# Performance work log

Hardware: AMD Instinct MI355X
Metric: run time of the kernel (lower is better)

The kernel has to match this reference:

```python
import jax, jax.numpy as jnp
import numpy as np

# config matching init_kwargs
C = 256; G = 16; GC = C // G; K = 3; P = K * K
PAD = 1; STR = 1; DIL = 1; OFFSET_SCALE = 1.0
N, H, W = 8, 64, 64


def setup_inputs() -> dict:
    key = jax.random.key(0)
    ks = jax.random.split(key, 8)
    def rn(k, shape, sc):
        return jax.random.normal(k, shape, jnp.float32) * sc
    return {
        "x": jax.random.normal(ks[0], (N, H, W, C), jnp.float32),
        "dw_w": rn(ks[1], (C, 1, K, K), 0.1),          # depthwise conv weight (OIHW, groups=C)
        "dw_b": jnp.zeros((C,), jnp.float32),
        "ln_g": jnp.ones((C,), jnp.float32),
        "ln_b": jnp.zeros((C,), jnp.float32),
        "off_w": rn(ks[2], (G * P * 2, C), 0.01),      # offset head (small so offsets stay sane)
        "off_b": jnp.zeros((G * P * 2,), jnp.float32),
        "mask_w": rn(ks[3], (G * P, C), 0.01),
        "mask_b": jnp.zeros((G * P,), jnp.float32),
        "in_w": rn(ks[4], (C, C), 0.05),
        "in_b": jnp.zeros((C,), jnp.float32),
        "out_w": rn(ks[5], (C, C), 0.05),
        "out_b": jnp.zeros((C,), jnp.float32),
    }


def _layer_norm(x, g, b, eps=1e-6):
    m = x.mean(-1, keepdims=True)
    v = ((x - m) ** 2).mean(-1, keepdims=True)
    return (x - m) * jax.lax.rsqrt(v + eps) * g + b


def _grid_sample_bilinear(img, grid):
    # img: (B, Cc, Hh, Ww); grid: (B, L, P, 2) normalized to [-1, 1], (x, y) order.
    # Matches torch.grid_sample(mode='bilinear', padding_mode='zeros', align_corners=False).
    B, Cc, Hh, Ww = img.shape
    gx = (grid[..., 0] + 1.0) * (Ww * 0.5) - 0.5
    gy = (grid[..., 1] + 1.0) * (Hh * 0.5) - 0.5
    x0 = jnp.floor(gx); y0 = jnp.floor(gy)
    tx = gx - x0; ty = gy - y0
    img_f = img.reshape(B, Cc, Hh * Ww)
    def corner(xi, yi, w):
        valid = (xi >= 0) & (xi < Ww) & (yi >= 0) & (yi < Hh)
        idx = (jnp.clip(yi, 0, Hh - 1) * Ww + jnp.clip(xi, 0, Ww - 1)).astype(jnp.int32)
        v = jnp.take_along_axis(img_f, idx.reshape(B, 1, -1), axis=2)  # (B, Cc, L*P)
        return v * (w * valid).reshape(B, 1, -1)
    out = (corner(x0, y0, (1 - tx) * (1 - ty)) + corner(x0 + 1, y0, tx * (1 - ty))
           + corner(x0, y0 + 1, (1 - tx) * ty) + corner(x0 + 1, y0 + 1, tx * ty))
    return out.reshape(B, Cc, grid.shape[1], grid.shape[2])  # (B, Cc, L, P)


def _dcnv3_core(x, offset, mask):
    # x: (N,H,W,C) value features; offset: (N,H,W,G*P*2); mask: (N,H,W,G*P)
    xpad = jnp.pad(x, ((0, 0), (PAD, PAD), (PAD, PAD), (0, 0)))
    Hi, Wi = H + 2 * PAD, W + 2 * PAD
    Ho, Wo = H, W
    # reference points (centers of receptive field), normalized by padded size
    start = (DIL * (K - 1)) // 2 + 0.5
    ry = (start + jnp.arange(Ho, dtype=jnp.float32) * STR) / Hi
    rx = (start + jnp.arange(Wo, dtype=jnp.float32) * STR) / Wi
    ref = jnp.stack([jnp.broadcast_to(rx[None, :], (Ho, Wo)),
                     jnp.broadcast_to(ry[:, None], (Ho, Wo))], -1)  # (Ho,Wo,2) (x,y)
    # dilation grid, x-major flattening to match torch meshgrid('ij') ordering
    d = jnp.arange(K, dtype=jnp.float32) * DIL - (DIL * (K - 1)) // 2
    kgrid = jnp.stack([jnp.repeat(d, K) / Wi, jnp.tile(d, K) / Hi], -1)  # (P,2)
    off = offset.reshape(N, Ho, Wo, G, P, 2)
    norm = jnp.array([Wi, Hi], jnp.float32)
    loc = (ref[None, :, :, None, None, :]
           + kgrid[None, None, None, None, :, :] * OFFSET_SCALE
           + off * OFFSET_SCALE / norm)                      # (N,Ho,Wo,G,P,2)
    sg = (2.0 * loc - 1.0).reshape(N, Ho * Wo, G, P, 2)
    sg = sg.transpose(0, 2, 1, 3, 4).reshape(N * G, Ho * Wo, P, 2)
    val = xpad.reshape(N, Hi * Wi, G * GC).transpose(0, 2, 1).reshape(N * G, GC, Hi, Wi)
    samp = _grid_sample_bilinear(val, sg)                    # (N*G, GC, Ho*Wo, P)
    m = mask.reshape(N, Ho * Wo, G, P).transpose(0, 2, 1, 3).reshape(N * G, 1, Ho * Wo, P)
    out = (samp * m).sum(-1)                                 # (N*G, GC, Ho*Wo)
    return out.reshape(N, G * GC, Ho * Wo).transpose(0, 2, 1).reshape(N, Ho, Wo, C)


def reference(x, dw_w, dw_b, ln_g, ln_b, off_w, off_b, mask_w, mask_b, in_w, in_b, out_w, out_b):
    xp = x @ in_w.T + in_b                                   # input_proj (values)
    # depthwise conv -> LN (channels_last) -> exact GELU
    y = jax.lax.conv_general_dilated(
        x.transpose(0, 3, 1, 2), dw_w, (1, 1), ((PAD, PAD), (PAD, PAD)),
        feature_group_count=C, dimension_numbers=('NCHW', 'OIHW', 'NCHW'))
    y = y + dw_b[None, :, None, None]
    x1 = jax.nn.gelu(_layer_norm(y.transpose(0, 2, 3, 1), ln_g, ln_b), approximate=False)
    offset = x1 @ off_w.T + off_b                            # (N,H,W,G*P*2)
    mlogits = (x1 @ mask_w.T + mask_b).reshape(N, H, W, G, P)
    mask = jax.nn.softmax(mlogits, axis=-1).reshape(N, H, W, G * P)
    out = _dcnv3_core(xp, offset, mask)
    return out @ out_w.T + out_b
```

## Files before the change

### kernel.cpp

```cpp
#include <hip/hip_runtime.h>


#define LL 32768
#define CC 256

typedef __bf16 bf16;
typedef __bf16 bf16x4 __attribute__((ext_vector_type(4)));
typedef __bf16 bf16x8 __attribute__((ext_vector_type(8)));
typedef float f32x4v __attribute__((ext_vector_type(4)));
typedef float f32x2 __attribute__((ext_vector_type(2)));

__device__ __forceinline__ void gload16(const bf16* g, const bf16* lds_base) {
    __builtin_amdgcn_global_load_lds(
        (const __attribute__((address_space(1))) void*)g,
        (__attribute__((address_space(3))) void*)lds_base, 16, 0, 0);
}

__global__ __launch_bounds__(256) void k_prep(
    const float* __restrict__ in_w, const float* __restrict__ off_w,
    const float* __restrict__ mask_w, const float* __restrict__ out_w,
    const float* __restrict__ dw_w, const float* __restrict__ off_b,
    const float* __restrict__ mask_b,
    bf16* __restrict__ in_h, bf16* __restrict__ hw_h,
    bf16* __restrict__ out_h,
    float* __restrict__ dwT, float* __restrict__ hbias) {
    int idx = blockIdx.x * 256 + threadIdx.x;
    if (idx < 60416) {
        const float* s; bf16* hi; int i;
        if (idx < 16384)      { s = in_w;   hi = in_h;          i = idx; }
        else if (idx < 34816) { s = off_w;  hi = hw_h;          i = idx - 16384; }
        else if (idx < 44032) { s = mask_w; hi = hw_h + 73728;  i = idx - 34816; }
        else                  { s = out_w;  hi = out_h;         i = idx - 44032; }
        float4 v = *(const float4*)(s + (size_t)i * 4);
        bf16x4 h;
        h[0] = (bf16)v.x; h[1] = (bf16)v.y; h[2] = (bf16)v.z; h[3] = (bf16)v.w;
        *(bf16x4*)(hi + (size_t)i * 4) = h;
    } else if (idx < 62720) {
        int e = idx - 60416;
        int c = e & 255, j = e >> 8;
        dwT[j * 256 + c] = dw_w[c * 9 + j];
    } else if (idx < 63232) {
        int e = idx - 62720;
        hbias[e] = (e < 288) ? off_b[e] : (e < 432 ? mask_b[e - 288] : 0.f);
    } else if (idx < 68352) {
        int e = idx - 63232;
        bf16x4 z = {(bf16)0.f, (bf16)0.f, (bf16)0.f, (bf16)0.f};
        *(bf16x4*)(hw_h + 110592 + (size_t)e * 4) = z;
    }
}

__global__ __launch_bounds__(256) void k_dwln(
    const float* __restrict__ x, const float* __restrict__ dwT,
    const float* __restrict__ dw_b, const float* __restrict__ ln_g,
    const float* __restrict__ ln_b, bf16* __restrict__ x1h,
    bf16* __restrict__ xb) {
    int t = threadIdx.x;
    int q = t >> 6, u = t & 63;
    int l = blockIdx.x * 4 + q;
    int w = l & 63, h = (l >> 6) & 63, n = l >> 12;
    int c0 = u * 4;

    float4 acc = *(const float4*)(dw_b + c0);
    float4 xc = {0.f, 0.f, 0.f, 0.f};
#pragma unroll
    for (int kh = 0; kh < 3; ++kh) {
        int hh = h + kh - 1;
        if (hh < 0 || hh >= 64) continue;
#pragma unroll
        for (int kw = 0; kw < 3; ++kw) {
            int ww = w + kw - 1;
            if (ww < 0 || ww >= 64) continue;
            float4 xv = *(const float4*)(x + (size_t)(((n * 64 + hh) * 64) + ww) * CC + c0);
            if (kh == 1 && kw == 1) xc = xv;
            float4 wv = *(const float4*)(dwT + (kh * 3 + kw) * 256 + c0);
            acc.x += xv.x * wv.x; acc.y += xv.y * wv.y;
            acc.z += xv.z * wv.z; acc.w += xv.w * wv.w;
        }
    }
    bf16x4 xcb;
    xcb[0] = (bf16)xc.x; xcb[1] = (bf16)xc.y;
    xcb[2] = (bf16)xc.z; xcb[3] = (bf16)xc.w;
    *(bf16x4*)(xb + (size_t)l * CC + c0) = xcb;

    float s = acc.x + acc.y + acc.z + acc.w;
    float ss = acc.x * acc.x + acc.y * acc.y + acc.z * acc.z + acc.w * acc.w;
#pragma unroll
    for (int d = 1; d < 64; d <<= 1) {
        s += __shfl_xor(s, d);
        ss += __shfl_xor(ss, d);
    }
    float mean = s * (1.0f / 256.0f);
    float var = ss * (1.0f / 256.0f) - mean * mean;
    float rstd = rsqrtf(var + 1e-6f);
    float4 gv = *(const float4*)(ln_g + c0);
    float4 bv = *(const float4*)(ln_b + c0);
    float xn0 = (acc.x - mean) * rstd * gv.x + bv.x;
    float xn1 = (acc.y - mean) * rstd * gv.y + bv.y;
    float xn2 = (acc.z - mean) * rstd * gv.z + bv.z;
    float xn3 = (acc.w - mean) * rstd * gv.w + bv.w;
    bf16x4 oh;
    oh[0] = (bf16)(0.5f * xn0 * (1.0f + erff(xn0 * 0.70710678118654752f)));
    oh[1] = (bf16)(0.5f * xn1 * (1.0f + erff(xn1 * 0.70710678118654752f)));
    oh[2] = (bf16)(0.5f * xn2 * (1.0f + erff(xn2 * 0.70710678118654752f)));
    oh[3] = (bf16)(0.5f * xn3 * (1.0f + erff(xn3 * 0.70710678118654752f)));
    *(bf16x4*)(x1h + (size_t)l * CC + c0) = oh;
}

template <bool OBF16>
__device__ __forceinline__ void gemm_core(
    const bf16* __restrict__ A, const bf16* __restrict__ Wh,
    const float* __restrict__ bias, float* __restrict__ C32,
    bf16* __restrict__ Cbf, int Nout, int mb, int nb) {
    int t = threadIdx.x, wave = t >> 6, lane = t & 63;
    int wm = wave & 1, wn = wave >> 1;
    int fm = lane & 15, fq = lane >> 4;

    __shared__ bf16 smem[16384];

    const bf16* gbase[4];
    int lofs[4];
#pragma unroll
    for (int j = 0; j < 4; ++j) {
        int seg = wave * 4 + j;
        int arr = seg >> 3;
        int row = (seg & 7) * 16 + (lane >> 2);
        int col = (lane & 3) * 8;
        gbase[j] = (arr == 0) ? (A + (size_t)(mb + row) * CC + col)
                              : (Wh + (size_t)(nb + row) * CC + col);
        lofs[j] = seg * 512;
    }

    f32x4v acc[4][4];
#pragma unroll
    for (int i = 0; i < 4; ++i)
#pragma unroll
        for (int j = 0; j < 4; ++j) acc[i][j] = (f32x4v){0.f, 0.f, 0.f, 0.f};

#pragma unroll
    for (int j = 0; j < 4; ++j) gload16(gbase[j], smem + lofs[j]);

    for (int kt = 0; kt < 8; ++kt) {
        const bf16* buf = smem + (kt & 1) * 8192;
        bf16* nxt = smem + ((kt & 1) ^ 1) * 8192;
        __syncthreads();
        if (kt < 7) {
#pragma unroll
            for (int j = 0; j < 4; ++j)
                gload16(gbase[j] + (kt + 1) * 32, nxt + lofs[j]);
        }
        bf16x8 af[4], bfh[4];
#pragma unroll
        for (int i = 0; i < 4; ++i)
            af[i] = *(const bf16x8*)&buf[(wm * 64 + i * 16 + fm) * 32 + fq * 8];
#pragma unroll
        for (int j = 0; j < 4; ++j)
            bfh[j] = *(const bf16x8*)&buf[4096 + (wn * 64 + j * 16 + fm) * 32 + fq * 8];
#pragma unroll
        for (int i = 0; i < 4; ++i)
#pragma unroll
            for (int j = 0; j < 4; ++j)
                acc[i][j] = __builtin_amdgcn_mfma_f32_16x16x32_bf16(
                    af[i], bfh[j], acc[i][j], 0, 0, 0);
    }

#pragma unroll
    for (int j = 0; j < 4; ++j) {
        int n_g = nb + wn * 64 + j * 16 + fm;
        if (n_g >= Nout) continue;
        float bv = bias[n_g];
#pragma unroll
        for (int i = 0; i < 4; ++i) {
            int m_g = mb + wm * 64 + i * 16 + fq * 4;
#pragma unroll
            for (int rg = 0; rg < 4; ++rg) {
                float o = acc[i][j][rg] + bv;
                if (OBF16)
                    Cbf[(size_t)(m_g + rg) * Nout + n_g] = (bf16)o;
                else
                    C32[(size_t)(m_g + rg) * Nout + n_g] = o;
            }
        }
    }
}

template <bool OBF16>
__global__ __launch_bounds__(256) void k_gemm(
    const bf16* __restrict__ A, const bf16* __restrict__ Wh,
    const float* __restrict__ bias, float* __restrict__ C32,
    bf16* __restrict__ Cbf, int Nout) {
    gemm_core<OBF16>(A, Wh, bias, C32, Cbf, Nout,
                     blockIdx.x * 128, blockIdx.y * 128);
}

__global__ __launch_bounds__(256) void k_gemm_ih(
    const bf16* __restrict__ xb, const bf16* __restrict__ x1h,
    const bf16* __restrict__ in_h, const bf16* __restrict__ hw_h,
    const float* __restrict__ in_b, const float* __restrict__ hbias,
    bf16* __restrict__ xpb, bf16* __restrict__ headb) {
    int mb = blockIdx.x * 128;
    int y = blockIdx.y;
    const bf16 *A, *W;
    const float* bs;
    bf16* Cb;
    int Nout, nb;
    if (y < 2) { A = xb;  W = in_h; bs = in_b;  Cb = xpb;   Nout = 256; nb = y * 128; }
    else       { A = x1h; W = hw_h; bs = hbias; Cb = headb; Nout = 432; nb = (y - 2) * 128; }
    gemm_core<true>(A, W, bs, nullptr, Cb, Nout, mb, nb);
}

__device__ __forceinline__ void mac8(f32x2 acc[4], bf16x8 v, float wt) {
    union { bf16x8 b; unsigned u[4]; } cu;
    cu.b = v;
    f32x2 wv = {wt, wt};
#pragma unroll
    for (int i = 0; i < 4; ++i) {
        f32x2 a;
        a.x = __uint_as_float(cu.u[i] << 16);
        a.y = __uint_as_float(cu.u[i] & 0xffff0000u);
        acc[i] += a * wv;
    }
}

__global__ __launch_bounds__(256) void k_gather(
    const bf16* __restrict__ xp, const bf16* __restrict__ head,
    bf16* __restrict__ rows) {
    int t = threadIdx.x;
    int q = t >> 5, u = t & 31;
    int l = blockIdx.x * 8 + q;
    int w = l & 63, h = (l >> 6) & 63, n = l >> 12;

    __shared__ float CW[8][576];
    __shared__ int BASE[8][144];

    for (int j = u; j < 432; j += 32) CW[q][j] = (float)head[(size_t)l * 432 + j];
    __syncthreads();

    if (u < 16) {
        int g = u;
        float mx = -1e30f;
#pragma unroll
        for (int p = 0; p < 9; ++p) mx = fmaxf(mx, CW[q][288 + g * 9 + p]);
        float s = 0.f, e[9];
#pragma unroll
        for (int p = 0; p < 9; ++p) { e[p] = expf(CW[q][288 + g * 9 + p] - mx); s += e[p]; }
        float inv = 1.0f / s;
#pragma unroll
        for (int p = 0; p < 9; ++p) CW[q][288 + g * 9 + p] = e[p] * inv;
    }
    __syncthreads();

    float4 cwr[5];
    int baser[5];
#pragma unroll
    for (int k = 0; k < 5; ++k) {
        if (k < 4 || u < 16) {
            int ei = u + 32 * k;
            int g = ei / 9, p = ei - g * 9;
            float ox = CW[q][g * 18 + p * 2 + 0];
            float oy = CW[q][g * 18 + p * 2 + 1];
            float m  = CW[q][288 + ei];
            float ax = (float)(w + (p / 3) - 1) + ox;
            float ay = (float)(h + (p % 3) - 1) + oy;
            float x0f = floorf(ax), y0f = floorf(ay);
            int x0 = (int)x0f, y0 = (int)y0f;
            float tx = ax - x0f, ty = ay - y0f;
            int xb, yb;
            float wxa, wxb, wya, wyb;
            if (x0 < 0)       { xb = 0;  wxa = (x0 == -1) ? tx : 0.f; wxb = 0.f; }
            else if (x0 > 62) { xb = 62; wxa = 0.f; wxb = (x0 == 63) ? (1.f - tx) : 0.f; }
            else              { xb = x0; wxa = 1.f - tx; wxb = tx; }
            if (y0 < 0)       { yb = 0;  wya = (y0 == -1) ? ty : 0.f; wyb = 0.f; }
            else if (y0 > 62) { yb = 62; wya = 0.f; wyb = (y0 == 63) ? (1.f - ty) : 0.f; }
            else              { yb = y0; wya = 1.f - ty; wyb = ty; }
            float4 cw;
            cw.x = m * wxa * wya; cw.y = m * wxb * wya;
            cw.z = m * wxa * wyb; cw.w = m * wxb * wyb;
            cwr[k] = cw;
            baser[k] = (n << 20) + (yb * 64 + xb) * 256;
        }
    }
    __syncthreads();
#pragma unroll
    for (int k = 0; k < 5; ++k) {
        if (k < 4 || u < 16) {
            int ei = u + 32 * k;
            *(float4*)&CW[q][ei * 4] = cwr[k];
            BASE[q][ei] = baser[k];
        }
    }
    __syncthreads();

    int g = u >> 1;
    int c0 = g * 16 + (u & 1) * 8;
    const bf16* xpc = xp + c0;
    f32x2 acc[4];
    acc[0] = (f32x2){0.f, 0.f}; acc[1] = (f32x2){0.f, 0.f};
    acc[2] = (f32x2){0.f, 0.f}; acc[3] = (f32x2){0.f, 0.f};
#pragma unroll
    for (int p = 0; p < 9; ++p) {
        int ei = g * 9 + p;
        float4 cw = *(const float4*)&CW[q][ei * 4];
        int base = BASE[q][ei];
        const bf16* p0 = xpc + base;
        const bf16* p1 = p0 + 16384;
        bf16x8 v00 = *(const bf16x8*)(p0);
        bf16x8 v01 = *(const bf16x8*)(p0 + 256);
        bf16x8 v10 = *(const bf16x8*)(p1);
        bf16x8 v11 = *(const bf16x8*)(p1 + 256);
        mac8(acc, v00, cw.x);
        mac8(acc, v01, cw.y);
        mac8(acc, v10, cw.z);
        mac8(acc, v11, cw.w);
    }
    bf16x8 oh;
    oh[0] = (bf16)acc[0].x; oh[1] = (bf16)acc[0].y;
    oh[2] = (bf16)acc[1].x; oh[3] = (bf16)acc[1].y;
    oh[4] = (bf16)acc[2].x; oh[5] = (bf16)acc[2].y;
    oh[6] = (bf16)acc[3].x; oh[7] = (bf16)acc[3].y;
    *(bf16x8*)(rows + (size_t)l * CC + c0) = oh;
}

__device__ __forceinline__ float dot256f(const float* a, const float* wrow) {
    const float4* w4 = (const float4*)wrow;
    float s = 0.f;
#pragma unroll 16
    for (int i = 0; i < 64; ++i) {
        float4 u = w4[i];
        const float* ap = a + i * 4;
        s += ap[0] * u.x + ap[1] * u.y + ap[2] * u.z + ap[3] * u.w;
    }
    return s;
}

__global__ __launch_bounds__(256) void k_inproj_fb(
    const float* __restrict__ x, const float* __restrict__ in_w,
    const float* __restrict__ in_b, float* __restrict__ xp) {
    int l = blockIdx.x;
    int t = threadIdx.x;
    __shared__ float xa[256];
    xa[t] = x[l * CC + t];
    __syncthreads();
    xp[l * CC + t] = dot256f(xa, in_w + t * CC) + in_b[t];
}

__device__ __forceinline__ float fetch_px_fb(const float* base, int yy, int xx) {
    if (xx < 0 || xx >= 64 || yy < 0 || yy >= 64) return 0.f;
    return base[(yy * 64 + xx) * CC];
}

__global__ __launch_bounds__(256) void k_main_fb(
    const float* __restrict__ x, const float* __restrict__ xp,
    const float* __restrict__ dw_w, const float* __restrict__ dw_b,
    const float* __restrict__ ln_g, const float* __restrict__ ln_b,
    const float* __restrict__ off_w, const float* __restrict__ off_b,
    const float* __restrict__ mask_w, const float* __restrict__ mask_b,
    const float* __restrict__ out_w, const float* __restrict__ out_b,
    float* __restrict__ out) {
    int l = blockIdx.x;
    int t = threadIdx.x;
    int w = l & 63, h = (l >> 6) & 63, n = l >> 12;
    __shared__ float x1[256];
    __shared__ float red[256];
    __shared__ float offs[288];
    __shared__ float ms[144];
    __shared__ float row[256];

    float acc = dw_b[t];
#pragma unroll
    for (int kh = 0; kh < 3; ++kh) {
        int hh = h + kh - 1;
        if (hh < 0 || hh >= 64) continue;
#pragma unroll
        for (int kw = 0; kw < 3; ++kw) {
            int ww = w + kw - 1;
            if (ww < 0 || ww >= 64) continue;
            acc += x[(((n * 64 + hh) * 64) + ww) * CC + t] * dw_w[t * 9 + kh * 3 + kw];
        }
    }
    red[t] = acc;
    __syncthreads();
    for (int s = 128; s > 0; s >>= 1) {
        if (t < s) red[t] += red[t + s];
        __syncthreads();
    }
    float mean = red[0] * (1.0f / 256.0f);
    __syncthreads();
    float d = acc - mean;
    red[t] = d * d;
    __syncthreads();
    for (int s = 128; s > 0; s >>= 1) {
        if (t < s) red[t] += red[t + s];
        __syncthreads();
    }
    float var = red[0] * (1.0f / 256.0f);
    float xn = d * rsqrtf(var + 1e-6f) * ln_g[t] + ln_b[t];
    x1[t] = 0.5f * xn * (1.0f + erff(xn * 0.70710678118654752f));
    __syncthreads();

    offs[t] = dot256f(x1, off_w + t * CC) + off_b[t];
    if (t < 32) {
        int j = 256 + t;
        offs[j] = dot256f(x1, off_w + j * CC) + off_b[j];
    }
    if (t < 144) ms[t] = dot256f(x1, mask_w + t * CC) + mask_b[t];
    __syncthreads();

    if (t < 16) {
        int g = t;
        float mx = -1e30f;
#pragma unroll
        for (int p = 0; p < 9; ++p) mx = fmaxf(mx, ms[g * 9 + p]);
        float s = 0.f, e[9];
#pragma unroll
        for (int p = 0; p < 9; ++p) { e[p] = expf(ms[g * 9 + p] - mx); s += e[p]; }
        float inv = 1.0f / s;
#pragma unroll
        for (int p = 0; p < 9; ++p) ms[g * 9 + p] = e[p] * inv;
    }
    __syncthreads();

    int g = t >> 4;
    const float* base = xp + (size_t)n * 64 * 64 * CC + t;
    float acc2 = 0.f;
#pragma unroll
    for (int p = 0; p < 9; ++p) {
        float ox = offs[g * 18 + p * 2 + 0];
        float oy = offs[g * 18 + p * 2 + 1];
        float ax = (float)(w + (p / 3) - 1) + ox;
        float ay = (float)(h + (p % 3) - 1) + oy;
        float x0f = floorf(ax), y0f = floorf(ay);
        int x0 = (int)x0f, y0 = (int)y0f;
        float tx = ax - x0f, ty = ay - y0f;
        float v00 = fetch_px_fb(base, y0, x0);
        float v01 = fetch_px_fb(base, y0, x0 + 1);
        float v10 = fetch_px_fb(base, y0 + 1, x0);
        float v11 = fetch_px_fb(base, y0 + 1, x0 + 1);
        float bl = (v00 * (1.f - tx) + v01 * tx) * (1.f - ty) +
                   (v10 * (1.f - tx) + v11 * tx) * ty;
        acc2 += ms[g * 9 + p] * bl;
    }
    row[t] = acc2;
    __syncthreads();
    out[l * CC + t] = dot256f(row, out_w + t * CC) + out_b[t];
}

extern "C" void kernel_launch(void* const* d_in, const int* in_sizes, int n_in,
                              void* d_out, int out_size, void* d_ws,
                              size_t ws_size, hipStream_t stream) {
    const float* x      = (const float*)d_in[0];
    const float* dw_w   = (const float*)d_in[1];
    const float* dw_b   = (const float*)d_in[2];
    const float* ln_g   = (const float*)d_in[3];
    const float* ln_b   = (const float*)d_in[4];
    const float* off_w  = (const float*)d_in[5];
    const float* off_b  = (const float*)d_in[6];
    const float* mask_w = (const float*)d_in[7];
    const float* mask_b = (const float*)d_in[8];
    const float* in_w   = (const float*)d_in[9];
    const float* in_b   = (const float*)d_in[10];
    const float* out_w  = (const float*)d_in[11];
    const float* out_b  = (const float*)d_in[12];
    float* out = (float*)d_out;

    const size_t szBF    = (size_t)LL * CC * 2;
    const size_t szHEADB = (size_t)LL * 432 * 2;
    const size_t szWB    = 1048576;
    const size_t need    = 3 * szBF + szHEADB + szWB;

    dim3 blk(256);
    if (ws_size >= need) {
        char* p = (char*)d_ws;
        bf16* x1h = (bf16*)p; p += szBF;
        bf16* xpb = (bf16*)p; p += szBF;
        bf16* xb  = (bf16*)p; p += szBF;
        bf16* headb = (bf16*)p; p += szHEADB;
        bf16* in_h  = (bf16*)p; p += 131072;
        bf16* hw_h  = (bf16*)p; p += 262144;
        bf16* out_h = (bf16*)p; p += 131072;
        float* dwT  = (float*)p; p += 9216;
        float* hbias = (float*)p;
        bf16* rows = x1h;

        k_prep<<<dim3(267), blk, 0, stream>>>(in_w, off_w, mask_w, out_w, dw_w,
                                              off_b, mask_b, in_h, hw_h, out_h,
                                              dwT, hbias);
        k_dwln<<<dim3(LL / 4), blk, 0, stream>>>(x, dwT, dw_b, ln_g, ln_b, x1h, xb);
        k_gemm_ih<<<dim3(256, 6), blk, 0, stream>>>(
            xb, x1h, in_h, hw_h, in_b, hbias, xpb, headb);
        k_gather<<<dim3(LL / 8), blk, 0, stream>>>(xpb, headb, rows);
        k_gemm<false><<<dim3(256, 2), blk, 0, stream>>>(
            rows, out_h, out_b, out, nullptr, 256);
    } else {
        float* xp = (float*)d_ws;
        k_inproj_fb<<<dim3(LL), blk, 0, stream>>>(x, in_w, in_b, xp);
        k_main_fb<<<dim3(LL), blk, 0, stream>>>(x, xp, dw_w, dw_b, ln_g, ln_b,
                                                off_w, off_b, mask_w, mask_b,
                                                out_w, out_b, out);
    }
}
```

Baseline: 199.1 us.

## Stage neighbourhood window of xp in LDS for deformable gather

Each gather block now copies a 6-row by 12-pixel window of the bf16 value tensor around its 8 output pixels into shared memory with global_load_lds. Bilinear samples whose corners fall inside this window are read from LDS; the rest fall back to global loads, flagged by bit-inverting the stored base offset. The head rows are also loaded as 16-byte vectors instead of scalars. The aim is to cut repeated global and L2 traffic for overlapping sample footprints, at the cost of roughly 36 KB more LDS per block, which lowers occupancy, plus window loads near image borders that can fall outside the buffer.

```diff
diff --git a/kernel.cpp b/kernel.cpp
--- a/kernel.cpp
+++ b/kernel.cpp
@@ -226,13 +226,42 @@
     bf16* __restrict__ rows) {
     int t = threadIdx.x;
     int q = t >> 5, u = t & 31;
-    int l = blockIdx.x * 8 + q;
+    int bl = blockIdx.x * 8;
+    int l = bl + q;
     int w = l & 63, h = (l >> 6) & 63, n = l >> 12;
-
+    int c0 = bl & 63;
+    int r  = (bl >> 6) & 63;
+    int nb = bl >> 12;
+
+    __shared__ bf16 WIN[18432];
     __shared__ float CW[8][576];
     __shared__ int BASE[8][144];
 
-    for (int j = u; j < 432; j += 32) CW[q][j] = (float)head[(size_t)l * 432 + j];
+    {
+        const char* xpB = (const char*)xp;
+        long long orig = (long long)((nb * 64 + (r - 2)) * 64 + (c0 - 2)) * 512;
+#pragma unroll
+        for (int j = 0; j < 9; ++j) {
+            int chunk = t + 256 * j;
+            int wr = chunk / 384;
+            int cx = chunk - wr * 384;
+            const char* src = xpB + orig + (long long)wr * 32768 + (long long)cx * 16;
+            gload16((const bf16*)src, WIN + chunk * 8);
+        }
+    }
+#pragma unroll
+    for (int jj = 0; jj < 2; ++jj) {
+        int cj = t + jj * 256;
+        if (cj < 432) {
+            int px = cj / 54, j = cj - px * 54;
+            bf16x8 v = *(const bf16x8*)(head + (size_t)(bl + px) * 432 + j * 8);
+            float4 f0, f1;
+            f0.x = (float)v[0]; f0.y = (float)v[1]; f0.z = (float)v[2]; f0.w = (float)v[3];
+            f1.x = (float)v[4]; f1.y = (float)v[5]; f1.z = (float)v[6]; f1.w = (float)v[7];
+            *(float4*)&CW[px][j * 8] = f0;
+            *(float4*)&CW[px][j * 8 + 4] = f1;
+        }
+    }
     __syncthreads();
 
     if (u < 16) {
@@ -264,19 +293,26 @@
             float x0f = floorf(ax), y0f = floorf(ay);
             int x0 = (int)x0f, y0 = (int)y0f;
             float tx = ax - x0f, ty = ay - y0f;
-            int xb, yb;
+            int xb_, yb_;
             float wxa, wxb, wya, wyb;
-            if (x0 < 0)       { xb = 0;  wxa = (x0 == -1) ? tx : 0.f; wxb = 0.f; }
-            else if (x0 > 62) { xb = 62; wxa = 0.f; wxb = (x0 == 63) ? (1.f - tx) : 0.f; }
-            else              { xb = x0; wxa = 1.f - tx; wxb = tx; }
-            if (y0 < 0)       { yb = 0;  wya = (y0 == -1) ? ty : 0.f; wyb = 0.f; }
-            else if (y0 > 62) { yb = 62; wya = 0.f; wyb = (y0 == 63) ? (1.f - ty) : 0.f; }
-            else              { yb = y0; wya = 1.f - ty; wyb = ty; }
+            if (x0 < 0)       { xb_ = 0;  wxa = (x0 == -1) ? tx : 0.f; wxb = 0.f; }
+            else if (x0 > 62) { xb_ = 62; wxa = 0.f; wxb = (x0 == 63) ? (1.f - tx) : 0.f; }
+            else              { xb_ = x0; wxa = 1.f - tx; wxb = tx; }
+            if (y0 < 0)       { yb_ = 0;  wya = (y0 == -1) ? ty : 0.f; wyb = 0.f; }
+            else if (y0 > 62) { yb_ = 62; wya = 0.f; wyb = (y0 == 63) ? (1.f - ty) : 0.f; }
+            else              { yb_ = y0; wya = 1.f - ty; wyb = ty; }
             float4 cw;
             cw.x = m * wxa * wya; cw.y = m * wxb * wya;
             cw.z = m * wxa * wyb; cw.w = m * wxb * wyb;
             cwr[k] = cw;
-            baser[k] = (n << 20) + (yb * 64 + xb) * 256;
+            bool inWin = (xb_ >= c0 - 2) & (xb_ <= c0 + 8) &
+                         (yb_ >= r - 2) & (yb_ <= r + 2);
+            if (inWin) {
+                int slot = (yb_ - (r - 2)) * 12 + (xb_ - (c0 - 2));
+                baser[k] = slot * 256 + g * 16;
+            } else {
+                baser[k] = ~((n << 20) + (yb_ * 64 + xb_) * 256);
+            }
         }
     }
     __syncthreads();
@@ -290,23 +326,34 @@
     }
     __syncthreads();
 
-    int g = u >> 1;
-    int c0 = g * 16 + (u & 1) * 8;
-    const bf16* xpc = xp + c0;
+    int g2 = u >> 1;
+    int half = u & 1;
+    int c0ch = g2 * 16 + half * 8;
+    const bf16* xpc = xp + c0ch;
     f32x2 acc[4];
     acc[0] = (f32x2){0.f, 0.f}; acc[1] = (f32x2){0.f, 0.f};
     acc[2] = (f32x2){0.f, 0.f}; acc[3] = (f32x2){0.f, 0.f};
 #pragma unroll
     for (int p = 0; p < 9; ++p) {
-        int ei = g * 9 + p;
+        int ei = g2 * 9 + p;
         float4 cw = *(const float4*)&CW[q][ei * 4];
-        int base = BASE[q][ei];
-        const bf16* p0 = xpc + base;
-        const bf16* p1 = p0 + 16384;
-        bf16x8 v00 = *(const bf16x8*)(p0);
-        bf16x8 v01 = *(const bf16x8*)(p0 + 256);
-        bf16x8 v10 = *(const bf16x8*)(p1);
-        bf16x8 v11 = *(const bf16x8*)(p1 + 256);
+        int b = BASE[q][ei];
+        bf16x8 v00, v01, v10, v11;
+        if (b >= 0) {
+            int e0 = b + half * 8;
+            v00 = *(const bf16x8*)&WIN[e0];
+            v01 = *(const bf16x8*)&WIN[e0 + 256];
+            v10 = *(const bf16x8*)&WIN[e0 + 3072];
+            v11 = *(const bf16x8*)&WIN[e0 + 3328];
+        } else {
+            int idxe = ~b;
+            const bf16* p0 = xpc + idxe;
+            const bf16* p1 = p0 + 16384;
+            v00 = *(const bf16x8*)(p0);
+            v01 = *(const bf16x8*)(p0 + 256);
+            v10 = *(const bf16x8*)(p1);
+            v11 = *(const bf16x8*)(p1 + 256);
+        }
         mac8(acc, v00, cw.x);
         mac8(acc, v01, cw.y);
         mac8(acc, v10, cw.z);
@@ -317,7 +364,7 @@
     oh[2] = (bf16)acc[1].x; oh[3] = (bf16)acc[1].y;
     oh[4] = (bf16)acc[2].x; oh[5] = (bf16)acc[2].y;
     oh[6] = (bf16)acc[3].x; oh[7] = (bf16)acc[3].y;
-    *(bf16x8*)(rows + (size_t)l * CC + c0) = oh;
+    *(bf16x8*)(rows + (size_t)l * CC + c0ch) = oh;
 }
 
 __device__ __forceinline__ float dot256f(const float* a, const float* wrow) {
```

Result: slower. 214.9 us (+8.0%).

## Store projected values in group-major layout for gather locality

Applied to the files above, without the earlier changes.

The input-projection GEMM now writes its bf16 output in a group-major layout (n, group, pixel, 16 channels) instead of pixel-major rows of 256 channels. The deformable gather kernel computes addresses in this layout, so a group's four bilinear corners sit in a compact 32-byte-per-pixel plane and neighbouring pixels are 32 bytes apart rather than 512. The aim is better cache-line and L2 locality for the random gathers. The cost is scattered 2-byte stores in the GEMM epilogue, which may write less efficiently.

```diff
diff --git a/kernel.cpp b/kernel.cpp
--- a/kernel.cpp
+++ b/kernel.cpp
@@ -106,7 +106,7 @@
     *(bf16x4*)(x1h + (size_t)l * CC + c0) = oh;
 }
 
-template <bool OBF16>
+template <bool OBF16, bool GM>
 __device__ __forceinline__ void gemm_core(
     const bf16* __restrict__ A, const bf16* __restrict__ Wh,
     const float* __restrict__ bias, float* __restrict__ C32,
@@ -174,10 +174,18 @@
 #pragma unroll
             for (int rg = 0; rg < 4; ++rg) {
                 float o = acc[i][j][rg] + bv;
-                if (OBF16)
-                    Cbf[(size_t)(m_g + rg) * Nout + n_g] = (bf16)o;
-                else
+                if (OBF16) {
+                    if (GM) {
+                        int mg = m_g + rg;
+                        size_t idx = ((size_t)((mg >> 12) * 16 + (n_g >> 4)) * 4096
+                                      + (mg & 4095)) * 16 + (n_g & 15);
+                        Cbf[idx] = (bf16)o;
+                    } else {
+                        Cbf[(size_t)(m_g + rg) * Nout + n_g] = (bf16)o;
+                    }
+                } else {
                     C32[(size_t)(m_g + rg) * Nout + n_g] = o;
+                }
             }
         }
     }
@@ -188,8 +196,8 @@
     const bf16* __restrict__ A, const bf16* __restrict__ Wh,
     const float* __restrict__ bias, float* __restrict__ C32,
     bf16* __restrict__ Cbf, int Nout) {
-    gemm_core<OBF16>(A, Wh, bias, C32, Cbf, Nout,
-                     blockIdx.x * 128, blockIdx.y * 128);
+    gemm_core<OBF16, false>(A, Wh, bias, C32, Cbf, Nout,
+                            blockIdx.x * 128, blockIdx.y * 128);
 }
 
 __global__ __launch_bounds__(256) void k_gemm_ih(
@@ -199,13 +207,11 @@
     bf16* __restrict__ xpb, bf16* __restrict__ headb) {
     int mb = blockIdx.x * 128;
     int y = blockIdx.y;
-    const bf16 *A, *W;
-    const float* bs;
-    bf16* Cb;
-    int Nout, nb;
-    if (y < 2) { A = xb;  W = in_h; bs = in_b;  Cb = xpb;   Nout = 256; nb = y * 128; }
-    else       { A = x1h; W = hw_h; bs = hbias; Cb = headb; Nout = 432; nb = (y - 2) * 128; }
-    gemm_core<true>(A, W, bs, nullptr, Cb, Nout, mb, nb);
+    if (y < 2)
+        gemm_core<true, true>(xb, in_h, in_b, nullptr, xpb, 256, mb, y * 128);
+    else
+        gemm_core<true, false>(x1h, hw_h, hbias, nullptr, headb, 432, mb,
+                               (y - 2) * 128);
 }
 
 __device__ __forceinline__ void mac8(f32x2 acc[4], bf16x8 v, float wt) {
@@ -276,7 +282,7 @@
             cw.x = m * wxa * wya; cw.y = m * wxb * wya;
             cw.z = m * wxa * wyb; cw.w = m * wxb * wyb;
             cwr[k] = cw;
-            baser[k] = (n << 20) + (yb * 64 + xb) * 256;
+            baser[k] = ((n * 16 + g) * 4096 + yb * 64 + xb) * 16;
         }
     }
     __syncthreads();
@@ -291,8 +297,8 @@
     __syncthreads();
 
     int g = u >> 1;
-    int c0 = g * 16 + (u & 1) * 8;
-    const bf16* xpc = xp + c0;
+    int half = u & 1;
+    int goff = half * 8;
     f32x2 acc[4];
     acc[0] = (f32x2){0.f, 0.f}; acc[1] = (f32x2){0.f, 0.f};
     acc[2] = (f32x2){0.f, 0.f}; acc[3] = (f32x2){0.f, 0.f};
@@ -300,13 +306,11 @@
     for (int p = 0; p < 9; ++p) {
         int ei = g * 9 + p;
         float4 cw = *(const float4*)&CW[q][ei * 4];
-        int base = BASE[q][ei];
-        const bf16* p0 = xpc + base;
-        const bf16* p1 = p0 + 16384;
+        const bf16* p0 = xp + BASE[q][ei] + goff;
         bf16x8 v00 = *(const bf16x8*)(p0);
-        bf16x8 v01 = *(const bf16x8*)(p0 + 256);
-        bf16x8 v10 = *(const bf16x8*)(p1);
-        bf16x8 v11 = *(const bf16x8*)(p1 + 256);
+        bf16x8 v01 = *(const bf16x8*)(p0 + 16);
+        bf16x8 v10 = *(const bf16x8*)(p0 + 1024);
+        bf16x8 v11 = *(const bf16x8*)(p0 + 1040);
         mac8(acc, v00, cw.x);
         mac8(acc, v01, cw.y);
         mac8(acc, v10, cw.z);
@@ -317,7 +321,7 @@
     oh[2] = (bf16)acc[1].x; oh[3] = (bf16)acc[1].y;
     oh[4] = (bf16)acc[2].x; oh[5] = (bf16)acc[2].y;
     oh[6] = (bf16)acc[3].x; oh[7] = (bf16)acc[3].y;
-    *(bf16x8*)(rows + (size_t)l * CC + c0) = oh;
+    *(bf16x8*)(rows + (size_t)l * CC + g * 16 + goff) = oh;
 }
 
 __device__ __forceinline__ float dot256f(const float* a, const float* wrow) {
```

Measured after the change: 212.3 us. +6.6%, slower.

## Fuse weight prep into depthwise-LN kernel and use smaller-M tile output GEMM

Applied to the files above, without the earlier changes.

Merges the weight-conversion prep kernel into the depthwise conv + LayerNorm kernel by appending extra blocks, which removes one launch and the dwT transpose. The conv now reads the OIHW depthwise weights directly with strided scalar loads. The final output GEMM moves to a dedicated kernel with 64x128 tiles, doubling the block count for better CU occupancy. Risks: the scalar strided weight loads are less coalesced than the old float4 reads from the transposed buffer, and the prep blocks now share the launch with the conv blocks.

```diff
diff --git a/kernel.cpp b/kernel.cpp
--- a/kernel.cpp
+++ b/kernel.cpp
@@ -16,52 +16,48 @@
         (__attribute__((address_space(3))) void*)lds_base, 16, 0, 0);
 }
 
-__global__ __launch_bounds__(256) void k_prep(
+__global__ __launch_bounds__(256) void k_dwp(
+    const float* __restrict__ x, const float* __restrict__ dw_w,
+    const float* __restrict__ dw_b, const float* __restrict__ ln_g,
+    const float* __restrict__ ln_b, bf16* __restrict__ x1h,
+    bf16* __restrict__ xb,
     const float* __restrict__ in_w, const float* __restrict__ off_w,
     const float* __restrict__ mask_w, const float* __restrict__ out_w,
-    const float* __restrict__ dw_w, const float* __restrict__ off_b,
-    const float* __restrict__ mask_b,
+    const float* __restrict__ off_b, const float* __restrict__ mask_b,
     bf16* __restrict__ in_h, bf16* __restrict__ hw_h,
-    bf16* __restrict__ out_h,
-    float* __restrict__ dwT, float* __restrict__ hbias) {
-    int idx = blockIdx.x * 256 + threadIdx.x;
-    if (idx < 60416) {
-        const float* s; bf16* hi; int i;
-        if (idx < 16384)      { s = in_w;   hi = in_h;          i = idx; }
-        else if (idx < 34816) { s = off_w;  hi = hw_h;          i = idx - 16384; }
-        else if (idx < 44032) { s = mask_w; hi = hw_h + 73728;  i = idx - 34816; }
-        else                  { s = out_w;  hi = out_h;         i = idx - 44032; }
-        float4 v = *(const float4*)(s + (size_t)i * 4);
-        bf16x4 h;
-        h[0] = (bf16)v.x; h[1] = (bf16)v.y; h[2] = (bf16)v.z; h[3] = (bf16)v.w;
-        *(bf16x4*)(hi + (size_t)i * 4) = h;
-    } else if (idx < 62720) {
-        int e = idx - 60416;
-        int c = e & 255, j = e >> 8;
-        dwT[j * 256 + c] = dw_w[c * 9 + j];
-    } else if (idx < 63232) {
-        int e = idx - 62720;
-        hbias[e] = (e < 288) ? off_b[e] : (e < 432 ? mask_b[e - 288] : 0.f);
-    } else if (idx < 68352) {
-        int e = idx - 63232;
-        bf16x4 z = {(bf16)0.f, (bf16)0.f, (bf16)0.f, (bf16)0.f};
-        *(bf16x4*)(hw_h + 110592 + (size_t)e * 4) = z;
-    }
-}
-
-__global__ __launch_bounds__(256) void k_dwln(
-    const float* __restrict__ x, const float* __restrict__ dwT,
-    const float* __restrict__ dw_b, const float* __restrict__ ln_g,
-    const float* __restrict__ ln_b, bf16* __restrict__ x1h,
-    bf16* __restrict__ xb) {
+    bf16* __restrict__ out_h, float* __restrict__ hbias) {
     int t = threadIdx.x;
+    int b = blockIdx.x;
+    if (b >= 8192) {
+        int idx = (b - 8192) * 256 + t;
+        if (idx < 60416) {
+            const float* s; bf16* hi; int i;
+            if (idx < 16384)      { s = in_w;   hi = in_h;          i = idx; }
+            else if (idx < 34816) { s = off_w;  hi = hw_h;          i = idx - 16384; }
+            else if (idx < 44032) { s = mask_w; hi = hw_h + 73728;  i = idx - 34816; }
+            else                  { s = out_w;  hi = out_h;         i = idx - 44032; }
+            float4 v = *(const float4*)(s + (size_t)i * 4);
+            bf16x4 hh;
+            hh[0] = (bf16)v.x; hh[1] = (bf16)v.y; hh[2] = (bf16)v.z; hh[3] = (bf16)v.w;
+            *(bf16x4*)(hi + (size_t)i * 4) = hh;
+        } else if (idx < 60928) {
+            int e = idx - 60416;
+            hbias[e] = (e < 288) ? off_b[e] : (e < 432 ? mask_b[e - 288] : 0.f);
+        } else {
+            int e = idx - 60928;
+            bf16x4 z = {(bf16)0.f, (bf16)0.f, (bf16)0.f, (bf16)0.f};
+            *(bf16x4*)(hw_h + 110592 + (size_t)e * 4) = z;
+        }
+        return;
+    }
     int q = t >> 6, u = t & 63;
-    int l = blockIdx.x * 4 + q;
+    int l = b * 4 + q;
     int w = l & 63, h = (l >> 6) & 63, n = l >> 12;
     int c0 = u * 4;
 
     float4 acc = *(const float4*)(dw_b + c0);
     float4 xc = {0.f, 0.f, 0.f, 0.f};
+    const float* wr0 = dw_w + (size_t)c0 * 9;
 #pragma unroll
     for (int kh = 0; kh < 3; ++kh) {
         int hh = h + kh - 1;
@@ -72,9 +68,11 @@
             if (ww < 0 || ww >= 64) continue;
             float4 xv = *(const float4*)(x + (size_t)(((n * 64 + hh) * 64) + ww) * CC + c0);
             if (kh == 1 && kw == 1) xc = xv;
-            float4 wv = *(const float4*)(dwT + (kh * 3 + kw) * 256 + c0);
-            acc.x += xv.x * wv.x; acc.y += xv.y * wv.y;
-            acc.z += xv.z * wv.z; acc.w += xv.w * wv.w;
+            int j = kh * 3 + kw;
+            acc.x += xv.x * wr0[j];
+            acc.y += xv.y * wr0[9 + j];
+            acc.z += xv.z * wr0[18 + j];
+            acc.w += xv.w * wr0[27 + j];
         }
     }
     bf16x4 xcb;
@@ -106,11 +104,10 @@
     *(bf16x4*)(x1h + (size_t)l * CC + c0) = oh;
 }
 
-template <bool OBF16>
 __device__ __forceinline__ void gemm_core(
     const bf16* __restrict__ A, const bf16* __restrict__ Wh,
-    const float* __restrict__ bias, float* __restrict__ C32,
-    bf16* __restrict__ Cbf, int Nout, int mb, int nb) {
+    const float* __restrict__ bias, bf16* __restrict__ Cbf,
+    int Nout, int mb, int nb) {
     int t = threadIdx.x, wave = t >> 6, lane = t & 63;
     int wm = wave & 1, wn = wave >> 1;
     int fm = lane & 15, fq = lane >> 4;
@@ -172,24 +169,10 @@
         for (int i = 0; i < 4; ++i) {
             int m_g = mb + wm * 64 + i * 16 + fq * 4;
 #pragma unroll
-            for (int rg = 0; rg < 4; ++rg) {
-                float o = acc[i][j][rg] + bv;
-                if (OBF16)
-                    Cbf[(size_t)(m_g + rg) * Nout + n_g] = (bf16)o;
-                else
-                    C32[(size_t)(m_g + rg) * Nout + n_g] = o;
-            }
-        }
-    }
-}
-
-template <bool OBF16>
-__global__ __launch_bounds__(256) void k_gemm(
-    const bf16* __restrict__ A, const bf16* __restrict__ Wh,
-    const float* __restrict__ bias, float* __restrict__ C32,
-    bf16* __restrict__ Cbf, int Nout) {
-    gemm_core<OBF16>(A, Wh, bias, C32, Cbf, Nout,
-                     blockIdx.x * 128, blockIdx.y * 128);
+            for (int rg = 0; rg < 4; ++rg)
+                Cbf[(size_t)(m_g + rg) * Nout + n_g] = (bf16)(acc[i][j][rg] + bv);
+        }
+    }
 }
 
 __global__ __launch_bounds__(256) void k_gemm_ih(
@@ -199,13 +182,80 @@
     bf16* __restrict__ xpb, bf16* __restrict__ headb) {
     int mb = blockIdx.x * 128;
     int y = blockIdx.y;
-    const bf16 *A, *W;
-    const float* bs;
-    bf16* Cb;
-    int Nout, nb;
-    if (y < 2) { A = xb;  W = in_h; bs = in_b;  Cb = xpb;   Nout = 256; nb = y * 128; }
-    else       { A = x1h; W = hw_h; bs = hbias; Cb = headb; Nout = 432; nb = (y - 2) * 128; }
-    gemm_core<true>(A, W, bs, nullptr, Cb, Nout, mb, nb);
+    if (y < 2)
+        gemm_core(xb, in_h, in_b, xpb, 256, mb, y * 128);
+    else
+        gemm_core(x1h, hw_h, hbias, headb, 432, mb, (y - 2) * 128);
+}
+
+__global__ __launch_bounds__(256) void k_gemm_out(
+    const bf16* __restrict__ A, const bf16* __restrict__ Wh,
+    const float* __restrict__ bias, float* __restrict__ C32) {
+    int mb = blockIdx.x * 64, nb = blockIdx.y * 128;
+    int t = threadIdx.x, wave = t >> 6, lane = t & 63;
+    int wm = wave & 1, wn = wave >> 1;
+    int fm = lane & 15, fq = lane >> 4;
+
+    __shared__ bf16 smem[12288];
+
+    const bf16* gbase[3];
+    int lofs[3];
+#pragma unroll
+    for (int j = 0; j < 3; ++j) {
+        int seg = wave * 3 + j;
+        int r16 = (seg < 4) ? seg : (seg - 4);
+        int row = r16 * 16 + (lane >> 2);
+        int col = (lane & 3) * 8;
+        gbase[j] = (seg < 4) ? (A + (size_t)(mb + row) * CC + col)
+                             : (Wh + (size_t)(nb + row) * CC + col);
+        lofs[j] = seg * 512;
+    }
+
+    f32x4v acc[2][4];
+#pragma unroll
+    for (int i = 0; i < 2; ++i)
+#pragma unroll
+        for (int j = 0; j < 4; ++j) acc[i][j] = (f32x4v){0.f, 0.f, 0.f, 0.f};
+
+#pragma unroll
+    for (int j = 0; j < 3; ++j) gload16(gbase[j], smem + lofs[j]);
+
+    for (int kt = 0; kt < 8; ++kt) {
+        const bf16* buf = smem + (kt & 1) * 6144;
+        bf16* nxt = smem + ((kt & 1) ^ 1) * 6144;
+        __syncthreads();
+        if (kt < 7) {
+#pragma unroll
+            for (int j = 0; j < 3; ++j)
+                gload16(gbase[j] + (kt + 1) * 32, nxt + lofs[j]);
+        }
+        bf16x8 af[2], bfh[4];
+#pragma unroll
+        for (int i = 0; i < 2; ++i)
+            af[i] = *(const bf16x8*)&buf[(wm * 32 + i * 16 + fm) * 32 + fq * 8];
+#pragma unroll
+        for (int j = 0; j < 4; ++j)
+            bfh[j] = *(const bf16x8*)&buf[2048 + (wn * 64 + j * 16 + fm) * 32 + fq * 8];
+#pragma unroll
+        for (int i = 0; i < 2; ++i)
+#pragma unroll
+            for (int j = 0; j < 4; ++j)
+                acc[i][j] = __builtin_amdgcn_mfma_f32_16x16x32_bf16(
+                    af[i], bfh[j], acc[i][j], 0, 0, 0);
+    }
+
+#pragma unroll
+    for (int j = 0; j < 4; ++j) {
+        int n_g = nb + wn * 64 + j * 16 + fm;
+        float bv = bias[n_g];
+#pragma unroll
+        for (int i = 0; i < 2; ++i) {
+            int m_g = mb + wm * 32 + i * 16 + fq * 4;
+#pragma unroll
+            for (int rg = 0; rg < 4; ++rg)
+                C32[(size_t)(m_g + rg) * 256 + n_g] = acc[i][j][rg] + bv;
+        }
+    }
 }
 
 __device__ __forceinline__ void mac8(f32x2 acc[4], bf16x8 v, float wt) {
@@ -477,19 +527,17 @@
         bf16* in_h  = (bf16*)p; p += 131072;
         bf16* hw_h  = (bf16*)p; p += 262144;
         bf16* out_h = (bf16*)p; p += 131072;
-        float* dwT  = (float*)p; p += 9216;
         float* hbias = (float*)p;
         bf16* rows = x1h;
 
-        k_prep<<<dim3(267), blk, 0, stream>>>(in_w, off_w, mask_w, out_w, dw_w,
-                                              off_b, mask_b, in_h, hw_h, out_h,
-                                              dwT, hbias);
-        k_dwln<<<dim3(LL / 4), blk, 0, stream>>>(x, dwT, dw_b, ln_g, ln_b, x1h, xb);
+        k_dwp<<<dim3(8450), blk, 0, stream>>>(
+            x, dw_w, dw_b, ln_g, ln_b, x1h, xb,
+            in_w, off_w, mask_w, out_w, off_b, mask_b,
+            in_h, hw_h, out_h, hbias);
         k_gemm_ih<<<dim3(256, 6), blk, 0, stream>>>(
             xb, x1h, in_h, hw_h, in_b, hbias, xpb, headb);
         k_gather<<<dim3(LL / 8), blk, 0, stream>>>(xpb, headb, rows);
-        k_gemm<false><<<dim3(256, 2), blk, 0, stream>>>(
-            rows, out_h, out_b, out, nullptr, 256);
+        k_gemm_out<<<dim3(512, 2), blk, 0, stream>>>(rows, out_h, out_b, out);
     } else {
         float* xp = (float*)d_ws;
         k_inproj_fb<<<dim3(LL), blk, 0, stream>>>(x, in_w, in_b, xp);
```

Result: slower. 246.7 us (+23.9%).
